# Performance work log

Measured on AMD Instinct MI355X. Metric: run time of the kernel, lower is better.

## Reference

```python
import jax, jax.numpy as jnp
import numpy as np

EPS = 1e-4
MAX_LAPLACE_VAR = 1000.0
MAX_DENSITY = 10000.0
BINS = 256

_LAP_KERNEL = jnp.array([[0., 1., 0.], [1., -4., 1.], [0., 1., 0.]], dtype=jnp.float32)[None, None]  # OIHW [1,1,3,3]


def setup_inputs() -> dict:
    key = jax.random.key(0)
    k1, k2 = jax.random.split(key)
    rgb_img = jax.random.uniform(k1, (32, 3, 512, 512), dtype=jnp.float32)
    depth_img = jax.random.normal(k2, (32, 1, 512, 512), dtype=jnp.float32)
    return {"rgb_img": rgb_img, "depth_img": depth_img}


def _rgb_confidence(rgb_img):
    B, C, H, W = rgb_img.shape
    gray = 0.299 * rgb_img[:, 0] + 0.587 * rgb_img[:, 1] + 0.114 * rgb_img[:, 2]  # [B,H,W]
    gray = gray[:, None]  # [B,1,H,W]
    lap = jax.lax.conv_general_dilated(
        gray, _LAP_KERNEL, window_strides=(1, 1), padding=[(1, 1), (1, 1)],
        dimension_numbers=("NCHW", "OIHW", "NCHW"))
    # torch.var default is unbiased (ddof=1)
    laplace_var = jnp.var(lap, axis=(1, 2, 3), ddof=1)

    # integer-valued pixels 0..255 land exactly in histc bins 0..255 (bins=256, min=0, max=255)
    vals = jnp.clip(gray * 255.0, 0.0, 255.0).astype(jnp.int32)  # [B,1,H,W]
    vals = vals.reshape(B, -1)  # [B, H*W]
    bidx = jnp.broadcast_to(jnp.arange(B)[:, None], vals.shape)
    hist = jnp.zeros((B, BINS), jnp.float32).at[bidx, vals].add(1.0)
    p = hist / jnp.sum(hist, axis=1, keepdims=True)
    entropy = -jnp.sum(p * jnp.log2(p + EPS), axis=1)

    clarity_score = laplace_var / (MAX_LAPLACE_VAR + EPS)
    uniformity_score = 1.0 / (entropy + EPS)
    return (0.5 * (clarity_score + uniformity_score))[:, None]  # [B,1]


def _depth_confidence(depth_img):
    C = depth_img.shape[1]
    depth_map = depth_img[:, 2] if C == 3 else depth_img[:, 0]  # [B,H,W]
    mask = (depth_map > 0).astype(jnp.float32)
    density = jnp.mean(mask, axis=(1, 2))

    # vectorized masked std (unbiased, ddof=1), matching torch.std over valid pixels
    n = jnp.sum(mask, axis=(1, 2))  # [B]
    mean = jnp.sum(depth_map * mask, axis=(1, 2)) / jnp.maximum(n, 1.0)
    sq = jnp.sum(mask * (depth_map - mean[:, None, None]) ** 2, axis=(1, 2))
    var = sq / jnp.maximum(n - 1.0, 1.0)
    std = jnp.sqrt(jnp.maximum(var, 0.0))
    noise_level = jnp.where(n > 0, std, 1.0)

    density_score = density / (MAX_DENSITY + EPS)
    noise_score = 1.0 / (noise_level + EPS)
    return (0.5 * (density_score + noise_score))[:, None]  # [B,1]


def reference(rgb_img, depth_img):
    rgb_conf = _rgb_confidence(rgb_img)
    depth_conf = _depth_confidence(depth_img)
    denom = rgb_conf + depth_conf + EPS
    w_r = rgb_conf / denom
    w_d = depth_conf / denom
    return (w_r, w_d)
```

## Files before the change

### kernel.cpp

```cpp
#include <hip/hip_runtime.h>

#define IMG_H 512
#define IMG_W 512
#define HW (IMG_H * IMG_W)
#define NB 32
#define ROWS 16
#define STRIPS (IMG_H / ROWS)

#define ACC_DOUBLES 160
#define WS_BYTES (ACC_DOUBLES * 8 + NB * 256 * 4)

__global__ __launch_bounds__(256, 4) void fused_kernel(
    const float* __restrict__ rgb, const float* __restrict__ depth,
    double* __restrict__ acc, unsigned int* __restrict__ hist)
{
    __shared__ float g[ROWS + 2][IMG_W];
    __shared__ unsigned int lh[256];
    __shared__ double red[4][5];

    const int t = threadIdx.x;
    const int b = blockIdx.y;
    const int s = blockIdx.x;
    const int row0 = s * ROWS;

    lh[t] = 0u;

    const float4* dp = (const float4*)(depth + (size_t)b * HW + (size_t)s * (HW / STRIPS));
    float4 dv[8];
    #pragma unroll
    for (int i = 0; i < 8; ++i) dv[i] = dp[i * 256 + t];

    const float* rp = rgb + (size_t)b * 3 * HW;
    const int half = t >> 7;
    const int c4 = (t & 127) << 2;
    #pragma unroll
    for (int j = 0; j < 9; ++j) {
        const int lr = 2 * j + half;
        const int gr = row0 + lr - 1;
        float4 gv = {0.f, 0.f, 0.f, 0.f};
        if (gr >= 0 && gr < IMG_H) {
            const size_t o = (size_t)gr * IMG_W + c4;
            const float4 r4 = *(const float4*)(rp + o);
            const float4 g4 = *(const float4*)(rp + HW + o);
            const float4 b4 = *(const float4*)(rp + 2 * HW + o);
            gv.x = 0.299f * r4.x + 0.587f * g4.x + 0.114f * b4.x;
            gv.y = 0.299f * r4.y + 0.587f * g4.y + 0.114f * b4.y;
            gv.z = 0.299f * r4.z + 0.587f * g4.z + 0.114f * b4.z;
            gv.w = 0.299f * r4.w + 0.587f * g4.w + 0.114f * b4.w;
        }
        *(float4*)&g[lr][c4] = gv;
    }

    float dnf = 0.f, dsf = 0.f, dqf = 0.f;
    #pragma unroll
    for (int i = 0; i < 8; ++i) {
        const float4 v = dv[i];
        if (v.x > 0.f) { dnf += 1.f; dsf += v.x; dqf += v.x * v.x; }
        if (v.y > 0.f) { dnf += 1.f; dsf += v.y; dqf += v.y * v.y; }
        if (v.z > 0.f) { dnf += 1.f; dsf += v.z; dqf += v.z * v.z; }
        if (v.w > 0.f) { dnf += 1.f; dsf += v.w; dqf += v.w * v.w; }
    }

    __syncthreads();

    float s1 = 0.f, s2 = 0.f;
    #pragma unroll
    for (int i = 0; i < 8; ++i) {
        const int gi = i * 256 + t;
        const int r = (gi >> 7) + 1;
        const int c = (gi & 127) << 2;
        const float4 ce = *(const float4*)&g[r][c];
        const float4 up = *(const float4*)&g[r - 1][c];
        const float4 dn = *(const float4*)&g[r + 1][c];
        const float lf = (c > 0) ? g[r][c - 1] : 0.f;
        const float rt = (c < IMG_W - 4) ? g[r][c + 4] : 0.f;
        float4 lap;
        lap.x = up.x + dn.x + lf   + ce.y - 4.f * ce.x;
        lap.y = up.y + dn.y + ce.x + ce.z - 4.f * ce.y;
        lap.z = up.z + dn.z + ce.y + ce.w - 4.f * ce.z;
        lap.w = up.w + dn.w + ce.z + rt   - 4.f * ce.w;
        s1 += lap.x + lap.y + lap.z + lap.w;
        s2 += lap.x * lap.x + lap.y * lap.y + lap.z * lap.z + lap.w * lap.w;
        atomicAdd(&lh[(int)fminf(fmaxf(ce.x * 255.f, 0.f), 255.f)], 1u);
        atomicAdd(&lh[(int)fminf(fmaxf(ce.y * 255.f, 0.f), 255.f)], 1u);
        atomicAdd(&lh[(int)fminf(fmaxf(ce.z * 255.f, 0.f), 255.f)], 1u);
        atomicAdd(&lh[(int)fminf(fmaxf(ce.w * 255.f, 0.f), 255.f)], 1u);
    }

    double z0 = (double)s1, z1 = (double)s2, z2 = (double)dnf, z3 = (double)dsf, z4 = (double)dqf;
    for (int off = 32; off > 0; off >>= 1) {
        z0 += __shfl_down(z0, off, 64);
        z1 += __shfl_down(z1, off, 64);
        z2 += __shfl_down(z2, off, 64);
        z3 += __shfl_down(z3, off, 64);
        z4 += __shfl_down(z4, off, 64);
    }
    const int wid = t >> 6, lane = t & 63;
    if (lane == 0) {
        red[wid][0] = z0; red[wid][1] = z1; red[wid][2] = z2;
        red[wid][3] = z3; red[wid][4] = z4;
    }
    __syncthreads();

    atomicAdd(&hist[b * 256 + t], lh[t]);
    if (t < 5) {
        const double v = red[0][t] + red[1][t] + red[2][t] + red[3][t];
        atomicAdd(&acc[t * 32 + b], v);
    }
}

__global__ __launch_bounds__(256) void final_kernel(
    const double* __restrict__ acc,
    const unsigned int* __restrict__ hist,
    float* __restrict__ out)
{
    __shared__ float part[256];
    const int t = threadIdx.x;
    const int b = t >> 3;
    const int sl = t & 7;
    float e = 0.f;
    #pragma unroll
    for (int i = 0; i < 32; ++i) {
        const float p = (float)hist[b * 256 + sl * 32 + i] * (1.0f / (float)HW);
        e += p * log2f(p + 1e-4f);
    }
    part[t] = e;
    __syncthreads();

    if (t < NB) {
        float es = 0.f;
        #pragma unroll
        for (int i = 0; i < 8; ++i) es += part[t * 8 + i];
        const double entropy = -(double)es;
        const double N = (double)HW;

        const double ls = acc[t], lq = acc[32 + t];
        const double lvar = (lq - ls * ls / N) / (N - 1.0);
        const double clarity = lvar / (1000.0 + 1e-4);
        const double uniformity = 1.0 / (entropy + 1e-4);
        const double rgb_conf = 0.5 * (clarity + uniformity);

        const double n = acc[64 + t], sdep = acc[96 + t], q = acc[128 + t];
        const double mean = sdep / fmax(n, 1.0);
        const double sq = q - 2.0 * mean * sdep + mean * mean * n;
        const double var = sq / fmax(n - 1.0, 1.0);
        const double stdd = sqrt(fmax(var, 0.0));
        const double noise = (n > 0.0) ? stdd : 1.0;
        const double density = n / N;
        const double depth_conf = 0.5 * (density / (10000.0 + 1e-4) + 1.0 / (noise + 1e-4));

        const double denom = rgb_conf + depth_conf + 1e-4;
        out[t]      = (float)(rgb_conf / denom);
        out[NB + t] = (float)(depth_conf / denom);
    }
}

extern "C" void kernel_launch(void* const* d_in, const int* in_sizes, int n_in,
                              void* d_out, int out_size, void* d_ws, size_t ws_size,
                              hipStream_t stream) {
    const float* rgb   = (const float*)d_in[0];
    const float* depth = (const float*)d_in[1];
    float* out = (float*)d_out;

    double* acc = (double*)d_ws;
    unsigned int* hist = (unsigned int*)((char*)d_ws + ACC_DOUBLES * 8);

    hipMemsetAsync(d_ws, 0, WS_BYTES, stream);

    fused_kernel<<<dim3(STRIPS, NB), 256, 0, stream>>>(rgb, depth, acc, hist);
    final_kernel<<<1, 256, 0, stream>>>(acc, hist, out);
}
```

Before: 192.8 us.

## Replace shared-memory stencil tile with register rolling-row Laplacian per wavefront

Drops the 18x512 shared gray tile. Each wavefront now owns 8 consecutive rows across the full width and keeps three rows of gray values in registers, getting horizontal neighbours through wave shuffles. Strips grow from 16 to 32 rows (512 blocks instead of 1024), which cuts halo reloads of RGB, and depth loads are interleaved into the row loop. The histogram is split into four per-wave shared copies to reduce atomic contention. In exchange there are fewer blocks, higher register pressure, and the explicit occupancy hint is removed.

```diff
diff --git a/kernel.cpp b/kernel.cpp
--- a/kernel.cpp
+++ b/kernel.cpp
@@ -4,87 +4,107 @@
 #define IMG_W 512
 #define HW (IMG_H * IMG_W)
 #define NB 32
-#define ROWS 16
-#define STRIPS (IMG_H / ROWS)
+#define STRIPS 16
+#define RPW 8
 
 #define ACC_DOUBLES 160
 #define WS_BYTES (ACC_DOUBLES * 8 + NB * 256 * 4)
 
-__global__ __launch_bounds__(256, 4) void fused_kernel(
+struct Row6 { float4 a0, a1, b0, b1, c0, c1; };
+
+__device__ inline Row6 load_row(const float* __restrict__ rp, int r, int c0) {
+    Row6 x;
+    if ((unsigned)r < IMG_H) {
+        const size_t o = (size_t)r * IMG_W + c0;
+        x.a0 = *(const float4*)(rp + o);
+        x.a1 = *(const float4*)(rp + o + 4);
+        x.b0 = *(const float4*)(rp + HW + o);
+        x.b1 = *(const float4*)(rp + HW + o + 4);
+        x.c0 = *(const float4*)(rp + 2 * HW + o);
+        x.c1 = *(const float4*)(rp + 2 * HW + o + 4);
+    } else {
+        const float4 z = {0.f, 0.f, 0.f, 0.f};
+        x.a0 = x.a1 = x.b0 = x.b1 = x.c0 = x.c1 = z;
+    }
+    return x;
+}
+
+__device__ inline void to_gray(const Row6& x, float g[8]) {
+    g[0] = 0.299f * x.a0.x + 0.587f * x.b0.x + 0.114f * x.c0.x;
+    g[1] = 0.299f * x.a0.y + 0.587f * x.b0.y + 0.114f * x.c0.y;
+    g[2] = 0.299f * x.a0.z + 0.587f * x.b0.z + 0.114f * x.c0.z;
+    g[3] = 0.299f * x.a0.w + 0.587f * x.b0.w + 0.114f * x.c0.w;
+    g[4] = 0.299f * x.a1.x + 0.587f * x.b1.x + 0.114f * x.c1.x;
+    g[5] = 0.299f * x.a1.y + 0.587f * x.b1.y + 0.114f * x.c1.y;
+    g[6] = 0.299f * x.a1.z + 0.587f * x.b1.z + 0.114f * x.c1.z;
+    g[7] = 0.299f * x.a1.w + 0.587f * x.b1.w + 0.114f * x.c1.w;
+}
+
+__global__ __launch_bounds__(256) void fused_kernel(
     const float* __restrict__ rgb, const float* __restrict__ depth,
     double* __restrict__ acc, unsigned int* __restrict__ hist)
 {
-    __shared__ float g[ROWS + 2][IMG_W];
-    __shared__ unsigned int lh[256];
+    __shared__ unsigned int lh[4][256];
     __shared__ double red[4][5];
 
     const int t = threadIdx.x;
     const int b = blockIdx.y;
     const int s = blockIdx.x;
-    const int row0 = s * ROWS;
+    const int lane = t & 63;
+    const int w = t >> 6;
 
-    lh[t] = 0u;
+    #pragma unroll
+    for (int i = 0; i < 4; ++i) lh[i][t & 255] = 0u;
+    __syncthreads();
+
+    const float* rp = rgb + (size_t)b * 3 * HW;
+    const int rb = s * 32 + w * RPW;
+    const int c0 = lane * 8;
 
     const float4* dp = (const float4*)(depth + (size_t)b * HW + (size_t)s * (HW / STRIPS));
-    float4 dv[8];
-    #pragma unroll
-    for (int i = 0; i < 8; ++i) dv[i] = dp[i * 256 + t];
 
-    const float* rp = rgb + (size_t)b * 3 * HW;
-    const int half = t >> 7;
-    const int c4 = (t & 127) << 2;
-    #pragma unroll
-    for (int j = 0; j < 9; ++j) {
-        const int lr = 2 * j + half;
-        const int gr = row0 + lr - 1;
-        float4 gv = {0.f, 0.f, 0.f, 0.f};
-        if (gr >= 0 && gr < IMG_H) {
-            const size_t o = (size_t)gr * IMG_W + c4;
-            const float4 r4 = *(const float4*)(rp + o);
-            const float4 g4 = *(const float4*)(rp + HW + o);
-            const float4 b4 = *(const float4*)(rp + 2 * HW + o);
-            gv.x = 0.299f * r4.x + 0.587f * g4.x + 0.114f * b4.x;
-            gv.y = 0.299f * r4.y + 0.587f * g4.y + 0.114f * b4.y;
-            gv.z = 0.299f * r4.z + 0.587f * g4.z + 0.114f * b4.z;
-            gv.w = 0.299f * r4.w + 0.587f * g4.w + 0.114f * b4.w;
-        }
-        *(float4*)&g[lr][c4] = gv;
-    }
-
-    float dnf = 0.f, dsf = 0.f, dqf = 0.f;
-    #pragma unroll
-    for (int i = 0; i < 8; ++i) {
-        const float4 v = dv[i];
-        if (v.x > 0.f) { dnf += 1.f; dsf += v.x; dqf += v.x * v.x; }
-        if (v.y > 0.f) { dnf += 1.f; dsf += v.y; dqf += v.y * v.y; }
-        if (v.z > 0.f) { dnf += 1.f; dsf += v.z; dqf += v.z * v.z; }
-        if (v.w > 0.f) { dnf += 1.f; dsf += v.w; dqf += v.w * v.w; }
-    }
-
-    __syncthreads();
+    float gp[8], gc[8], gn[8];
+    Row6 st0 = load_row(rp, rb - 1, c0);
+    Row6 st1 = load_row(rp, rb, c0);
+    to_gray(st0, gp);
+    to_gray(st1, gc);
 
     float s1 = 0.f, s2 = 0.f;
+    float dnf = 0.f, dsf = 0.f, dqf = 0.f;
+
     #pragma unroll
-    for (int i = 0; i < 8; ++i) {
-        const int gi = i * 256 + t;
-        const int r = (gi >> 7) + 1;
-        const int c = (gi & 127) << 2;
-        const float4 ce = *(const float4*)&g[r][c];
-        const float4 up = *(const float4*)&g[r - 1][c];
-        const float4 dn = *(const float4*)&g[r + 1][c];
-        const float lf = (c > 0) ? g[r][c - 1] : 0.f;
-        const float rt = (c < IMG_W - 4) ? g[r][c + 4] : 0.f;
-        float4 lap;
-        lap.x = up.x + dn.x + lf   + ce.y - 4.f * ce.x;
-        lap.y = up.y + dn.y + ce.x + ce.z - 4.f * ce.y;
-        lap.z = up.z + dn.z + ce.y + ce.w - 4.f * ce.z;
-        lap.w = up.w + dn.w + ce.z + rt   - 4.f * ce.w;
-        s1 += lap.x + lap.y + lap.z + lap.w;
-        s2 += lap.x * lap.x + lap.y * lap.y + lap.z * lap.z + lap.w * lap.w;
-        atomicAdd(&lh[(int)fminf(fmaxf(ce.x * 255.f, 0.f), 255.f)], 1u);
-        atomicAdd(&lh[(int)fminf(fmaxf(ce.y * 255.f, 0.f), 255.f)], 1u);
-        atomicAdd(&lh[(int)fminf(fmaxf(ce.z * 255.f, 0.f), 255.f)], 1u);
-        atomicAdd(&lh[(int)fminf(fmaxf(ce.w * 255.f, 0.f), 255.f)], 1u);
+    for (int r = 0; r < RPW; ++r) {
+        const Row6 nx = load_row(rp, rb + r + 1, c0);
+        const float4 d0 = dp[(2 * r) * 256 + t];
+        const float4 d1 = dp[(2 * r + 1) * 256 + t];
+        to_gray(nx, gn);
+
+        float lf = __shfl_up(gc[7], 1, 64);
+        if (lane == 0) lf = 0.f;
+        float rt = __shfl_down(gc[0], 1, 64);
+        if (lane == 63) rt = 0.f;
+
+        #pragma unroll
+        for (int j = 0; j < 8; ++j) {
+            const float left  = (j == 0) ? lf : gc[j - 1];
+            const float right = (j == 7) ? rt : gc[j + 1];
+            const float lap = gp[j] + gn[j] + left + right - 4.f * gc[j];
+            s1 += lap;
+            s2 += lap * lap;
+            atomicAdd(&lh[w][(int)fminf(fmaxf(gc[j] * 255.f, 0.f), 255.f)], 1u);
+        }
+
+        if (d0.x > 0.f) { dnf += 1.f; dsf += d0.x; dqf += d0.x * d0.x; }
+        if (d0.y > 0.f) { dnf += 1.f; dsf += d0.y; dqf += d0.y * d0.y; }
+        if (d0.z > 0.f) { dnf += 1.f; dsf += d0.z; dqf += d0.z * d0.z; }
+        if (d0.w > 0.f) { dnf += 1.f; dsf += d0.w; dqf += d0.w * d0.w; }
+        if (d1.x > 0.f) { dnf += 1.f; dsf += d1.x; dqf += d1.x * d1.x; }
+        if (d1.y > 0.f) { dnf += 1.f; dsf += d1.y; dqf += d1.y * d1.y; }
+        if (d1.z > 0.f) { dnf += 1.f; dsf += d1.z; dqf += d1.z * d1.z; }
+        if (d1.w > 0.f) { dnf += 1.f; dsf += d1.w; dqf += d1.w * d1.w; }
+
+        #pragma unroll
+        for (int j = 0; j < 8; ++j) { gp[j] = gc[j]; gc[j] = gn[j]; }
     }
 
     double z0 = (double)s1, z1 = (double)s2, z2 = (double)dnf, z3 = (double)dsf, z4 = (double)dqf;
@@ -95,14 +115,13 @@
         z3 += __shfl_down(z3, off, 64);
         z4 += __shfl_down(z4, off, 64);
     }
-    const int wid = t >> 6, lane = t & 63;
     if (lane == 0) {
-        red[wid][0] = z0; red[wid][1] = z1; red[wid][2] = z2;
-        red[wid][3] = z3; red[wid][4] = z4;
+        red[w][0] = z0; red[w][1] = z1; red[w][2] = z2; red[w][3] = z3; red[w][4] = z4;
     }
     __syncthreads();
 
-    atomicAdd(&hist[b * 256 + t], lh[t]);
+    const unsigned int hsum = lh[0][t] + lh[1][t] + lh[2][t] + lh[3][t];
+    atomicAdd(&hist[b * 256 + t], hsum);
     if (t < 5) {
         const double v = red[0][t] + red[1][t] + red[2][t] + red[3][t];
         atomicAdd(&acc[t * 32 + b], v);
```

New measurement: 178.8 us. -7.3%, faster.

## Replace global atomics and memset with per-strip partials and per-image final reduction

Applied to the files above, without the earlier changes.

Each block now writes its per-strip histogram and five moment sums to separate workspace slots, so the global atomics and the memset launch go away. The final kernel runs one block per image and reduces the strip partials there. The histogram is built during the load loop using two per-wave-pair shared copies to reduce LDS atomic contention, and the depth loads are interleaved with the rgb loads. The cost is a larger partial buffer to write and read back, plus more work in the final kernel.

```diff
diff --git a/kernel.cpp b/kernel.cpp
--- a/kernel.cpp
+++ b/kernel.cpp
@@ -4,42 +4,39 @@
 #define IMG_W 512
 #define HW (IMG_H * IMG_W)
 #define NB 32
-#define ROWS 16
-#define STRIPS (IMG_H / ROWS)
+#define STRIPS 32
+#define SROWS 16
 
-#define ACC_DOUBLES 160
-#define WS_BYTES (ACC_DOUBLES * 8 + NB * 256 * 4)
+#define ACC_OFF (NB * STRIPS * 256 * 4)
 
-__global__ __launch_bounds__(256, 4) void fused_kernel(
+__global__ __launch_bounds__(256, 4) void stream_kernel(
     const float* __restrict__ rgb, const float* __restrict__ depth,
-    double* __restrict__ acc, unsigned int* __restrict__ hist)
+    unsigned int* __restrict__ hist_part, double* __restrict__ acc_part)
 {
-    __shared__ float g[ROWS + 2][IMG_W];
-    __shared__ unsigned int lh[256];
+    __shared__ float gray[SROWS + 2][IMG_W];
+    __shared__ unsigned int lh[2][256];
     __shared__ double red[4][5];
 
     const int t = threadIdx.x;
     const int b = blockIdx.y;
     const int s = blockIdx.x;
-    const int row0 = s * ROWS;
+    const int lane = t & 63;
+    const int w = t >> 6;
 
-    lh[t] = 0u;
-
-    const float4* dp = (const float4*)(depth + (size_t)b * HW + (size_t)s * (HW / STRIPS));
-    float4 dv[8];
-    #pragma unroll
-    for (int i = 0; i < 8; ++i) dv[i] = dp[i * 256 + t];
+    lh[0][t] = 0u;
+    lh[1][t] = 0u;
+    __syncthreads();
 
     const float* rp = rgb + (size_t)b * 3 * HW;
-    const int half = t >> 7;
-    const int c4 = (t & 127) << 2;
-    #pragma unroll
-    for (int j = 0; j < 9; ++j) {
-        const int lr = 2 * j + half;
-        const int gr = row0 + lr - 1;
+    const float4* dp = (const float4*)(depth + (size_t)b * HW) + s * 2048;
+
+    {
+        const int hr = (w < 2) ? (SROWS * s - 1) : (SROWS * s + SROWS);
+        const int lr = (w < 2) ? 0 : (SROWS + 1);
+        const int c4 = (w < 2) ? t : (t - 128);
         float4 gv = {0.f, 0.f, 0.f, 0.f};
-        if (gr >= 0 && gr < IMG_H) {
-            const size_t o = (size_t)gr * IMG_W + c4;
+        if ((unsigned)hr < IMG_H) {
+            const size_t o = (size_t)hr * IMG_W + 4 * c4;
             const float4 r4 = *(const float4*)(rp + o);
             const float4 g4 = *(const float4*)(rp + HW + o);
             const float4 b4 = *(const float4*)(rp + 2 * HW + o);
@@ -48,17 +45,34 @@
             gv.z = 0.299f * r4.z + 0.587f * g4.z + 0.114f * b4.z;
             gv.w = 0.299f * r4.w + 0.587f * g4.w + 0.114f * b4.w;
         }
-        *(float4*)&g[lr][c4] = gv;
+        *(float4*)&gray[lr][4 * c4] = gv;
     }
 
     float dnf = 0.f, dsf = 0.f, dqf = 0.f;
     #pragma unroll
     for (int i = 0; i < 8; ++i) {
-        const float4 v = dv[i];
-        if (v.x > 0.f) { dnf += 1.f; dsf += v.x; dqf += v.x * v.x; }
-        if (v.y > 0.f) { dnf += 1.f; dsf += v.y; dqf += v.y * v.y; }
-        if (v.z > 0.f) { dnf += 1.f; dsf += v.z; dqf += v.z * v.z; }
-        if (v.w > 0.f) { dnf += 1.f; dsf += v.w; dqf += v.w * v.w; }
+        const int p = i * 256 + t;
+        const int r = p >> 7;
+        const int c4 = p & 127;
+        const size_t o = (size_t)(SROWS * s + r) * IMG_W + 4 * c4;
+        const float4 r4 = *(const float4*)(rp + o);
+        const float4 g4 = *(const float4*)(rp + HW + o);
+        const float4 b4 = *(const float4*)(rp + 2 * HW + o);
+        const float4 d4 = dp[p];
+        float4 gv;
+        gv.x = 0.299f * r4.x + 0.587f * g4.x + 0.114f * b4.x;
+        gv.y = 0.299f * r4.y + 0.587f * g4.y + 0.114f * b4.y;
+        gv.z = 0.299f * r4.z + 0.587f * g4.z + 0.114f * b4.z;
+        gv.w = 0.299f * r4.w + 0.587f * g4.w + 0.114f * b4.w;
+        *(float4*)&gray[r + 1][4 * c4] = gv;
+        atomicAdd(&lh[w & 1][(int)fminf(fmaxf(gv.x * 255.f, 0.f), 255.f)], 1u);
+        atomicAdd(&lh[w & 1][(int)fminf(fmaxf(gv.y * 255.f, 0.f), 255.f)], 1u);
+        atomicAdd(&lh[w & 1][(int)fminf(fmaxf(gv.z * 255.f, 0.f), 255.f)], 1u);
+        atomicAdd(&lh[w & 1][(int)fminf(fmaxf(gv.w * 255.f, 0.f), 255.f)], 1u);
+        if (d4.x > 0.f) { dnf += 1.f; dsf += d4.x; dqf += d4.x * d4.x; }
+        if (d4.y > 0.f) { dnf += 1.f; dsf += d4.y; dqf += d4.y * d4.y; }
+        if (d4.z > 0.f) { dnf += 1.f; dsf += d4.z; dqf += d4.z * d4.z; }
+        if (d4.w > 0.f) { dnf += 1.f; dsf += d4.w; dqf += d4.w * d4.w; }
     }
 
     __syncthreads();
@@ -66,14 +80,14 @@
     float s1 = 0.f, s2 = 0.f;
     #pragma unroll
     for (int i = 0; i < 8; ++i) {
-        const int gi = i * 256 + t;
-        const int r = (gi >> 7) + 1;
-        const int c = (gi & 127) << 2;
-        const float4 ce = *(const float4*)&g[r][c];
-        const float4 up = *(const float4*)&g[r - 1][c];
-        const float4 dn = *(const float4*)&g[r + 1][c];
-        const float lf = (c > 0) ? g[r][c - 1] : 0.f;
-        const float rt = (c < IMG_W - 4) ? g[r][c + 4] : 0.f;
+        const int p = i * 256 + t;
+        const int r = p >> 7;
+        const int c = 4 * (p & 127);
+        const float4 up = *(const float4*)&gray[r][c];
+        const float4 ce = *(const float4*)&gray[r + 1][c];
+        const float4 dn = *(const float4*)&gray[r + 2][c];
+        const float lf = (c > 0) ? gray[r + 1][c - 1] : 0.f;
+        const float rt = (c < IMG_W - 4) ? gray[r + 1][c + 4] : 0.f;
         float4 lap;
         lap.x = up.x + dn.x + lf   + ce.y - 4.f * ce.x;
         lap.y = up.y + dn.y + ce.x + ce.z - 4.f * ce.y;
@@ -81,10 +95,6 @@
         lap.w = up.w + dn.w + ce.z + rt   - 4.f * ce.w;
         s1 += lap.x + lap.y + lap.z + lap.w;
         s2 += lap.x * lap.x + lap.y * lap.y + lap.z * lap.z + lap.w * lap.w;
-        atomicAdd(&lh[(int)fminf(fmaxf(ce.x * 255.f, 0.f), 255.f)], 1u);
-        atomicAdd(&lh[(int)fminf(fmaxf(ce.y * 255.f, 0.f), 255.f)], 1u);
-        atomicAdd(&lh[(int)fminf(fmaxf(ce.z * 255.f, 0.f), 255.f)], 1u);
-        atomicAdd(&lh[(int)fminf(fmaxf(ce.w * 255.f, 0.f), 255.f)], 1u);
     }
 
     double z0 = (double)s1, z1 = (double)s2, z2 = (double)dnf, z3 = (double)dsf, z4 = (double)dqf;
@@ -95,52 +105,67 @@
         z3 += __shfl_down(z3, off, 64);
         z4 += __shfl_down(z4, off, 64);
     }
-    const int wid = t >> 6, lane = t & 63;
     if (lane == 0) {
-        red[wid][0] = z0; red[wid][1] = z1; red[wid][2] = z2;
-        red[wid][3] = z3; red[wid][4] = z4;
+        red[w][0] = z0; red[w][1] = z1; red[w][2] = z2; red[w][3] = z3; red[w][4] = z4;
     }
     __syncthreads();
 
-    atomicAdd(&hist[b * 256 + t], lh[t]);
+    hist_part[(b * STRIPS + s) * 256 + t] = lh[0][t] + lh[1][t];
     if (t < 5) {
-        const double v = red[0][t] + red[1][t] + red[2][t] + red[3][t];
-        atomicAdd(&acc[t * 32 + b], v);
+        acc_part[(b * STRIPS + s) * 5 + t] =
+            red[0][t] + red[1][t] + red[2][t] + red[3][t];
     }
 }
 
 __global__ __launch_bounds__(256) void final_kernel(
-    const double* __restrict__ acc,
-    const unsigned int* __restrict__ hist,
+    const unsigned int* __restrict__ hist_part,
+    const double* __restrict__ acc_part,
     float* __restrict__ out)
 {
-    __shared__ float part[256];
+    __shared__ double epart[4];
+    __shared__ double asum[5];
+
     const int t = threadIdx.x;
-    const int b = t >> 3;
-    const int sl = t & 7;
-    float e = 0.f;
+    const int b = blockIdx.x;
+    const int lane = t & 63;
+    const int w = t >> 6;
+
+    const unsigned int* hp = hist_part + b * STRIPS * 256;
+    unsigned int tot = 0;
     #pragma unroll
-    for (int i = 0; i < 32; ++i) {
-        const float p = (float)hist[b * 256 + sl * 32 + i] * (1.0f / (float)HW);
-        e += p * log2f(p + 1e-4f);
+    for (int st = 0; st < STRIPS; ++st) tot += hp[st * 256 + t];
+    const float p = (float)tot * (1.0f / (float)HW);
+    double ed = (double)(p * log2f(p + 1e-4f));
+    for (int off = 32; off > 0; off >>= 1) ed += __shfl_down(ed, off, 64);
+    if (lane == 0) epart[w] = ed;
+
+    if (w == 0) {
+        double a[5];
+        #pragma unroll
+        for (int k = 0; k < 5; ++k)
+            a[k] = (lane < STRIPS) ? acc_part[(b * STRIPS + lane) * 5 + k] : 0.0;
+        for (int off = 32; off > 0; off >>= 1) {
+            #pragma unroll
+            for (int k = 0; k < 5; ++k) a[k] += __shfl_down(a[k], off, 64);
+        }
+        if (lane == 0) {
+            #pragma unroll
+            for (int k = 0; k < 5; ++k) asum[k] = a[k];
+        }
     }
-    part[t] = e;
     __syncthreads();
 
-    if (t < NB) {
-        float es = 0.f;
-        #pragma unroll
-        for (int i = 0; i < 8; ++i) es += part[t * 8 + i];
-        const double entropy = -(double)es;
+    if (t == 0) {
+        const double entropy = -(epart[0] + epart[1] + epart[2] + epart[3]);
         const double N = (double)HW;
 
-        const double ls = acc[t], lq = acc[32 + t];
+        const double ls = asum[0], lq = asum[1];
         const double lvar = (lq - ls * ls / N) / (N - 1.0);
         const double clarity = lvar / (1000.0 + 1e-4);
         const double uniformity = 1.0 / (entropy + 1e-4);
         const double rgb_conf = 0.5 * (clarity + uniformity);
 
-        const double n = acc[64 + t], sdep = acc[96 + t], q = acc[128 + t];
+        const double n = asum[2], sdep = asum[3], q = asum[4];
         const double mean = sdep / fmax(n, 1.0);
         const double sq = q - 2.0 * mean * sdep + mean * mean * n;
         const double var = sq / fmax(n - 1.0, 1.0);
@@ -150,8 +175,8 @@
         const double depth_conf = 0.5 * (density / (10000.0 + 1e-4) + 1.0 / (noise + 1e-4));
 
         const double denom = rgb_conf + depth_conf + 1e-4;
-        out[t]      = (float)(rgb_conf / denom);
-        out[NB + t] = (float)(depth_conf / denom);
+        out[b]      = (float)(rgb_conf / denom);
+        out[NB + b] = (float)(depth_conf / denom);
     }
 }
 
@@ -162,11 +187,9 @@
     const float* depth = (const float*)d_in[1];
     float* out = (float*)d_out;
 
-    double* acc = (double*)d_ws;
-    unsigned int* hist = (unsigned int*)((char*)d_ws + ACC_DOUBLES * 8);
+    unsigned int* hist_part = (unsigned int*)d_ws;
+    double* acc_part = (double*)((char*)d_ws + ACC_OFF);
 
-    hipMemsetAsync(d_ws, 0, WS_BYTES, stream);
-
-    fused_kernel<<<dim3(STRIPS, NB), 256, 0, stream>>>(rgb, depth, acc, hist);
-    final_kernel<<<1, 256, 0, stream>>>(acc, hist, out);
+    stream_kernel<<<dim3(STRIPS, NB), 256, 0, stream>>>(rgb, depth, hist_part, acc_part);
+    final_kernel<<<NB, 256, 0, stream>>>(hist_part, acc_part, out);
 }
```

Result: faster. 188.4 us (-2.3%).
